# Kernel tuning notes

Hardware: AMD Instinct MI355X
Metric: run time of the kernel (lower is better)

Reference implementation:

```python
import jax, jax.numpy as jnp
import numpy as np

H, D = 8, 16          # heads, head dim -> out_channels = 128
L = 3                 # num GATv2 layers per graph stack
NUM_GRAPHS = 128      # pooled batch size
NEG_SLOPE = 0.2       # GATv2 leaky_relu slope


def _gatv2_stack(x, edge_index, eattr, linlW, linlb, linrW, linrb, lineW, att, bias, resW, resb):
    # x: [N, C]; edge_index: [2, E]; eattr: [E, edge_dim]
    src, dst = edge_index[0], edge_index[1]
    N = x.shape[0]
    for l in range(L):
        xl = (x @ linlW[l] + linlb[l]).reshape(N, H, D)   # source transform
        xr = (x @ linrW[l] + linrb[l]).reshape(N, H, D)   # target transform
        em = (eattr @ lineW[l]).reshape(-1, H, D)         # edge transform
        m = jax.nn.leaky_relu(xl[src] + xr[dst] + em, NEG_SLOPE)   # [E, H, D]
        logits = jnp.einsum('ehd,hd->eh', m, att[l])                # [E, H]
        # segment softmax over destination nodes (numerically stable)
        lmax = jax.ops.segment_max(logits, dst, num_segments=N)
        lmax = jnp.where(jnp.isfinite(lmax), lmax, 0.0)
        ex = jnp.exp(logits - lmax[dst])
        denom = jax.ops.segment_sum(ex, dst, num_segments=N)
        alpha = ex / (denom[dst] + 1e-16)
        agg = jax.ops.segment_sum(alpha[..., None] * xl[src], dst, num_segments=N)
        h = agg.reshape(N, H * D) + bias[l]               # GATv2Conv output
        x = h + jax.nn.elu(h @ resW[l] + resb[l])         # residual Linear+ELU block
    return x


def reference(mg_x, pg_x, mg_eattr, pg_eattr,
              mg_linlW, mg_linlb, mg_linrW, mg_linrb, mg_lineW, mg_att, mg_bias, mg_resW, mg_resb,
              pg_linlW, pg_linlb, pg_linrW, pg_linrb, pg_lineW, pg_att, pg_bias, pg_resW, pg_resb,
              fc1W, fc1b, fc2W, fc2b,
              mg_edge_index, pg_edge_index, mg_batch, pg_batch):
    mg_h = _gatv2_stack(mg_x, mg_edge_index, mg_eattr, mg_linlW, mg_linlb, mg_linrW, mg_linrb,
                        mg_lineW, mg_att, mg_bias, mg_resW, mg_resb)
    pg_h = _gatv2_stack(pg_x, pg_edge_index, pg_eattr, pg_linlW, pg_linlb, pg_linrW, pg_linrb,
                        pg_lineW, pg_att, pg_bias, pg_resW, pg_resb)
    mg_pool = jax.ops.segment_sum(mg_h, mg_batch, num_segments=NUM_GRAPHS)  # global_add_pool
    pg_pool = jax.ops.segment_sum(pg_h, pg_batch, num_segments=NUM_GRAPHS)
    z = jnp.concatenate([mg_pool, pg_pool], axis=-1)      # [B, 256]
    z = jax.nn.elu(z @ fc1W + fc1b)
    return jax.nn.sigmoid(z @ fc2W + fc2b)                # [B, 1]


def setup_inputs() -> dict:
    key = jax.random.key(0)
    ks = jax.random.split(key, 24)
    NM, NP = 50000, 20000          # molecule / protein node counts
    EM, EP = 400000, 400000        # edge counts
    EDM, EDP = 8, 12               # edge feature dims
    C = H * D                      # 128 = out_channels
    s = 0.05
    rn = lambda k, sh: jax.random.normal(k, sh, dtype=jnp.float32)
    return {
        "mg_x": rn(ks[0], (NM, C)),
        "pg_x": rn(ks[1], (NP, C)),
        "mg_eattr": rn(ks[2], (EM, EDM)),
        "pg_eattr": rn(ks[3], (EP, EDP)),
        "mg_linlW": rn(ks[4], (L, C, C)) * s,
        "mg_linlb": jnp.zeros((L, C), jnp.float32),
        "mg_linrW": rn(ks[5], (L, C, C)) * s,
        "mg_linrb": jnp.zeros((L, C), jnp.float32),
        "mg_lineW": rn(ks[6], (L, EDM, C)) * s,
        "mg_att": rn(ks[7], (L, H, D)) * s,
        "mg_bias": jnp.zeros((L, C), jnp.float32),
        "mg_resW": rn(ks[8], (L, C, C)) * s,
        "mg_resb": jnp.zeros((L, C), jnp.float32),
        "pg_linlW": rn(ks[9], (L, C, C)) * s,
        "pg_linlb": jnp.zeros((L, C), jnp.float32),
        "pg_linrW": rn(ks[10], (L, C, C)) * s,
        "pg_linrb": jnp.zeros((L, C), jnp.float32),
        "pg_lineW": rn(ks[11], (L, EDP, C)) * s,
        "pg_att": rn(ks[12], (L, H, D)) * s,
        "pg_bias": jnp.zeros((L, C), jnp.float32),
        "pg_resW": rn(ks[13], (L, C, C)) * s,
        "pg_resb": jnp.zeros((L, C), jnp.float32),
        "fc1W": rn(ks[14], (2 * C, C)) * s,
        "fc1b": jnp.zeros((C,), jnp.float32),
        "fc2W": rn(ks[15], (C, 1)) * s,
        "fc2b": jnp.zeros((1,), jnp.float32),
        "mg_edge_index": jax.random.randint(ks[16], (2, EM), 0, NM, dtype=jnp.int32),
        "pg_edge_index": jax.random.randint(ks[17], (2, EP), 0, NP, dtype=jnp.int32),
        "mg_batch": jnp.sort(jax.random.randint(ks[18], (NM,), 0, NUM_GRAPHS, dtype=jnp.int32)),
        "pg_batch": jnp.sort(jax.random.randint(ks[19], (NP,), 0, NUM_GRAPHS, dtype=jnp.int32)),
    }
```

## Files before the change

kernel.cpp:

```cpp
#include <hip/hip_runtime.h>
#include <hip/hip_bf16.h>

#define CDIM 128
#define NG 128
typedef unsigned int uint32;
typedef unsigned short ushort16;
typedef __attribute__((ext_vector_type(8))) short short8;
typedef __attribute__((ext_vector_type(4))) float floatx4;

__device__ __forceinline__ ushort16 f2bf(float f){
  uint32 u = __float_as_uint(f);
  u = (u + 0x7fffu + ((u >> 16) & 1u)) >> 16;
  return (ushort16)u;
}

__global__ void k_count_f(const int* __restrict__ dstM, const int* __restrict__ dstP,
                          int* __restrict__ deg, int EM, int ET, int NM){
  int e = blockIdx.x*blockDim.x + threadIdx.x;
  if (e < ET){
    int d = (e < EM) ? dstM[e] : dstP[e-EM] + NM;
    atomicAdd(&deg[d], 1);
  }
}

__global__ void k_scan1(const int* __restrict__ deg, int* __restrict__ rowptr,
                        int* __restrict__ sums, int N){
  __shared__ int tmp[1024];
  int b = blockIdx.x, t = threadIdx.x;
  int i = b*1024 + t;
  int v = (i < N) ? deg[i] : 0;
  tmp[t] = v; __syncthreads();
  for (int off = 1; off < 1024; off <<= 1){
    int a = (t >= off) ? tmp[t-off] : 0;
    __syncthreads();
    tmp[t] += a;
    __syncthreads();
  }
  if (i < N) rowptr[i] = tmp[t] - v;
  if (t == 1023) sums[b] = tmp[t];
}

__global__ void k_scan2(int* __restrict__ sums, int nb){
  __shared__ int tmp[1024];
  __shared__ int carry;
  int t = threadIdx.x;
  if (t == 0) carry = 0;
  __syncthreads();
  for (int base = 0; base < nb; base += 1024){
    int i = base + t;
    int v = (i < nb) ? sums[i] : 0;
    tmp[t] = v; __syncthreads();
    for (int off = 1; off < 1024; off <<= 1){
      int a = (t >= off) ? tmp[t-off] : 0;
      __syncthreads();
      tmp[t] += a;
      __syncthreads();
    }
    if (i < nb) sums[i] = carry + tmp[t] - v;
    int tot = tmp[1023];
    __syncthreads();
    if (t == 0) carry += tot;
    __syncthreads();
  }
  if (t == 0) sums[nb] = carry;
}

__global__ void k_scan3(int* __restrict__ rowptr, int* __restrict__ cursor,
                        const int* __restrict__ sums, int N, int nb){
  int i = blockIdx.x*blockDim.x + threadIdx.x;
  if (i < N){
    int r = rowptr[i] + sums[i >> 10];
    rowptr[i] = r; cursor[i] = r;
  }
  if (i == 0) rowptr[N] = sums[nb];
}

__global__ void k_scatter_f(const int* __restrict__ srcM, const int* __restrict__ srcP,
                            const int* __restrict__ dstM, const int* __restrict__ dstP,
                            int* __restrict__ cursor, int* __restrict__ csr_src,
                            int* __restrict__ csr_eid, int EM, int ET, int NM){
  int e = blockIdx.x*blockDim.x + threadIdx.x;
  if (e < ET){
    int s, d;
    if (e < EM){ s = srcM[e]; d = dstM[e]; }
    else       { s = srcP[e-EM] + NM; d = dstP[e-EM] + NM; }
    int pos = atomicAdd(&cursor[d], 1);
    csr_src[pos] = s;
    csr_eid[pos] = e;
  }
}

__global__ void k_reorder_f(const float* __restrict__ eaM, const float* __restrict__ eaP,
                            const int* __restrict__ eid, float* __restrict__ ea_csr,
                            int EM, int ET, int edM, int edP, int edmax){
  int i = blockIdx.x*blockDim.x + threadIdx.x;
  if (i >= ET*edmax) return;
  int j = i/edmax, k = i - j*edmax;
  if (j < EM){
    if (k < edM) ea_csr[(size_t)j*edM + k] = eaM[(size_t)eid[j]*edM + k];
  } else {
    if (k < edP) ea_csr[(size_t)EM*edM + (size_t)(j-EM)*edP + k]
                 = eaP[(size_t)(eid[j]-EM)*edP + k];
  }
}

__global__ void k_prep_w(const float* __restrict__ linlW_M, const float* __restrict__ linrW_M,
                         const float* __restrict__ resW_M,
                         const float* __restrict__ linlW_P, const float* __restrict__ linrW_P,
                         const float* __restrict__ resW_P,
                         ushort16* __restrict__ WtAll, ushort16* __restrict__ resWt){
  const int per = 256*CDIM + CDIM*CDIM;
  int idx = blockIdx.x*blockDim.x + threadIdx.x;
  if (idx >= 6*per) return;
  int sl = idx / per; int rem = idx - sl*per;
  int s = sl / 3, l = sl % 3;
  const float* Wl = (s ? linlW_P : linlW_M) + (size_t)l*CDIM*CDIM;
  const float* Wr = (s ? linrW_P : linrW_M) + (size_t)l*CDIM*CDIM;
  const float* Rw = (s ? resW_P  : resW_M ) + (size_t)l*CDIM*CDIM;
  if (rem < 256*CDIM){
    int k = rem >> 8, n = rem & 255;
    float v = (n < CDIM) ? Wl[k*CDIM + n] : Wr[k*CDIM + (n-CDIM)];
    WtAll[((size_t)sl*256 + n)*CDIM + k] = f2bf(v);
  } else {
    int r2 = rem - 256*CDIM;
    int k = r2 >> 7, n = r2 & 127;
    resWt[((size_t)sl*CDIM + n)*CDIM + k] = f2bf(Rw[k*CDIM + n]);
  }
}

__global__ void __launch_bounds__(256, 6)
k_transform_mfma(const float* __restrict__ xM, const float* __restrict__ xP,
    const ushort16* __restrict__ WtM, const ushort16* __restrict__ WtP,
    const float* __restrict__ blM, const float* __restrict__ brM,
    const float* __restrict__ blP, const float* __restrict__ brP,
    ushort16* __restrict__ xlh, float* __restrict__ xr,
    int NM, int nb32M, int NP)
{
  __shared__ ushort16 xs[32*CDIM];
  __shared__ float   xro[32*CDIM];
  int tid = threadIdx.x;
  int b = blockIdx.x;
  const float* xin; const ushort16* Wt; const float *bl, *br;
  int n0, nn, outbase;
  if (b < nb32M){ xin=xM; n0=b*32; nn=min(32,NM-n0); outbase=n0; Wt=WtM; bl=blM; br=brM; }
  else { xin=xP; n0=(b-nb32M)*32; nn=min(32,NP-n0); outbase=NM+n0; Wt=WtP; bl=blP; br=brP; }
  for (int i = 0; i < 16; i++){
    int e = tid + i*256;
    int row = e >> 7, col = e & 127;
    float v = (row < nn) ? xin[(size_t)(n0+row)*CDIM + col] : 0.f;
    int byte = (row*256 + col*2) ^ ((row & 7) << 4);
    *(ushort16*)((char*)xs + byte) = f2bf(v);
  }
  __syncthreads();
  int w = tid >> 6, t = tid & 63;
  int r16 = t & 15, kg = t >> 4;
  floatx4 acc[2][4];
  #pragma unroll
  for (int m = 0; m < 2; m++)
    #pragma unroll
    for (int nb = 0; nb < 4; nb++) acc[m][nb] = (floatx4){0.f,0.f,0.f,0.f};
  #pragma unroll
  for (int ks = 0; ks < 4; ks++){
    short8 a[2];
    #pragma unroll
    for (int m = 0; m < 2; m++){
      int row = m*16 + r16;
      int byte = (row*256 + ks*64 + kg*16) ^ ((row & 7) << 4);
      a[m] = *(const short8*)((const char*)xs + byte);
    }
    #pragma unroll
    for (int nb = 0; nb < 4; nb++){
      int col = w*64 + nb*16 + r16;
      short8 bf = *(const short8*)(Wt + (size_t)col*CDIM + ks*32 + kg*8);
      #pragma unroll
      for (int m = 0; m < 2; m++)
        acc[m][nb] = __builtin_amdgcn_mfma_f32_16x16x32_bf16(a[m], bf, acc[m][nb], 0, 0, 0);
    }
  }
  __syncthreads();
  #pragma unroll
  for (int nb = 0; nb < 4; nb++){
    int col = w*64 + nb*16 + r16;
    float bias = (col < CDIM) ? bl[col] : br[col - CDIM];
    #pragma unroll
    for (int m = 0; m < 2; m++){
      #pragma unroll
      for (int reg = 0; reg < 4; reg++){
        int row = m*16 + kg*4 + reg;
        float v = acc[m][nb][reg] + bias;
        if (col < CDIM) xs[row*CDIM + col] = f2bf(v);
        else            xro[row*CDIM + (col - CDIM)] = v;
      }
    }
  }
  __syncthreads();
  for (int i = 0; i < 16; i++){
    int e = tid + i*256;
    int row = e >> 7, col = e & 127;
    if (row < nn){
      xlh[(size_t)(outbase+row)*CDIM + col] = xs[e];
      xr [(size_t)(outbase+row)*CDIM + col] = xro[e];
    }
  }
}

template<int ED>
__device__ __forceinline__ void gat_edges(
    int start, int end, int t, int j0, int ed_rt,
    const uint32* __restrict__ xlu, float2 xrv, float2 at2,
    const float2* __restrict__ lw2,
    const float* __restrict__ ea, const int* __restrict__ eid,
    const int* __restrict__ csr_src,
    float& m, float& den, float& a0, float& a1)
{
  const int ed = (ED > 0) ? ED : ed_rt;
  for (int j = start; j < end; j += 4){
    const int r = end - j;
    int jj1 = (1 < r) ? j+1 : j;
    int jj2 = (2 < r) ? j+2 : j;
    int jj3 = (3 < r) ? j+3 : j;
    int s0 = __builtin_amdgcn_readfirstlane(csr_src[j]);
    int s1 = __builtin_amdgcn_readfirstlane(csr_src[jj1]);
    int s2 = __builtin_amdgcn_readfirstlane(csr_src[jj2]);
    int s3 = __builtin_amdgcn_readfirstlane(csr_src[jj3]);
    int e0 = __builtin_amdgcn_readfirstlane((eid ? eid[j]   : j)   - j0);
    int e1 = __builtin_amdgcn_readfirstlane((eid ? eid[jj1] : jj1) - j0);
    int e2 = __builtin_amdgcn_readfirstlane((eid ? eid[jj2] : jj2) - j0);
    int e3 = __builtin_amdgcn_readfirstlane((eid ? eid[jj3] : jj3) - j0);
    const float* p0 = ea + (size_t)e0*ed;
    const float* p1 = ea + (size_t)e1*ed;
    const float* p2 = ea + (size_t)e2*ed;
    const float* p3 = ea + (size_t)e3*ed;
    uint32 u0 = xlu[(size_t)s0*64 + t];
    uint32 u1 = xlu[(size_t)s1*64 + t];
    uint32 u2 = xlu[(size_t)s2*64 + t];
    uint32 u3 = xlu[(size_t)s3*64 + t];
    float x0x = __uint_as_float(u0 << 16), x0y = __uint_as_float(u0 & 0xffff0000u);
    float x1x = __uint_as_float(u1 << 16), x1y = __uint_as_float(u1 & 0xffff0000u);
    float x2x = __uint_as_float(u2 << 16), x2y = __uint_as_float(u2 & 0xffff0000u);
    float x3x = __uint_as_float(u3 << 16), x3y = __uint_as_float(u3 & 0xffff0000u);
    float em00=0.f, em01=0.f, em10=0.f, em11=0.f;
    float em20=0.f, em21=0.f, em30=0.f, em31=0.f;
    #pragma unroll 4
    for (int k = 0; k < ed; k++){
      float2 lwv = lw2[k*64 + t];
      float a = p0[k], bq = p1[k], c = p2[k], d = p3[k];
      em00 = fmaf(a,  lwv.x, em00); em01 = fmaf(a,  lwv.y, em01);
      em10 = fmaf(bq, lwv.x, em10); em11 = fmaf(bq, lwv.y, em11);
      em20 = fmaf(c,  lwv.x, em20); em21 = fmaf(c,  lwv.y, em21);
      em30 = fmaf(d,  lwv.x, em30); em31 = fmaf(d,  lwv.y, em31);
    }
    float m00 = x0x + xrv.x + em00; m00 = (m00>=0.f)?m00:0.2f*m00;
    float m01 = x0y + xrv.y + em01; m01 = (m01>=0.f)?m01:0.2f*m01;
    float m10 = x1x + xrv.x + em10; m10 = (m10>=0.f)?m10:0.2f*m10;
    float m11 = x1y + xrv.y + em11; m11 = (m11>=0.f)?m11:0.2f*m11;
    float m20 = x2x + xrv.x + em20; m20 = (m20>=0.f)?m20:0.2f*m20;
    float m21 = x2y + xrv.y + em21; m21 = (m21>=0.f)?m21:0.2f*m21;
    float m30 = x3x + xrv.x + em30; m30 = (m30>=0.f)?m30:0.2f*m30;
    float m31 = x3y + xrv.y + em31; m31 = (m31>=0.f)?m31:0.2f*m31;
    float v0 = fmaf(m00, at2.x, m01*at2.y);
    float v1 = fmaf(m10, at2.x, m11*at2.y);
    float v2 = fmaf(m20, at2.x, m21*at2.y);
    float v3 = fmaf(m30, at2.x, m31*at2.y);
    #pragma unroll
    for (int off = 1; off < 8; off <<= 1){
      v0 += __shfl_xor(v0, off, 8);
      v1 += __shfl_xor(v1, off, 8);
      v2 += __shfl_xor(v2, off, 8);
      v3 += __shfl_xor(v3, off, 8);
    }
    if (1 >= r) v1 = -INFINITY;
    if (2 >= r) v2 = -INFINITY;
    if (3 >= r) v3 = -INFINITY;
    float vmax = fmaxf(fmaxf(v0, v1), fmaxf(v2, v3));
    if (vmax > m + 8.f){
      float sc = __expf(m - vmax);
      den *= sc; a0 *= sc; a1 *= sc; m = vmax;
    }
    float w0 = __expf(v0 - m), w1 = __expf(v1 - m);
    float w2 = __expf(v2 - m), w3 = __expf(v3 - m);
    den += (w0 + w1) + (w2 + w3);
    a0 = fmaf(w0, x0x, fmaf(w1, x1x, fmaf(w2, x2x, fmaf(w3, x3x, a0))));
    a1 = fmaf(w0, x0y, fmaf(w1, x1y, fmaf(w2, x2y, fmaf(w3, x3y, a1))));
  }
}

template<int EDM_T, int EDP_T>
__global__ void __launch_bounds__(256, 8)
k_gat_f(const uint32* __restrict__ xlu, const float2* __restrict__ xr2,
    const float* __restrict__ eaM, const float* __restrict__ eaP,
    const int* __restrict__ eid,
    const float* __restrict__ lwM, const float* __restrict__ atM, const float* __restrict__ biM,
    const float* __restrict__ lwP, const float* __restrict__ atP, const float* __restrict__ biP,
    const int* __restrict__ rowptr, const int* __restrict__ csr_src,
    float2* __restrict__ hout2, int NM, int NT, int EM, int edM_rt, int edP_rt)
{
  const int edM = (EDM_T > 0) ? EDM_T : edM_rt;
  const int edP = (EDP_T > 0) ? EDP_T : edP_rt;
  __shared__ float lw[24*CDIM];
  int tb = threadIdx.x;
  for (int i = tb; i < edM*CDIM; i += 256) lw[i] = lwM[i];
  for (int i = tb; i < edP*CDIM; i += 256) lw[edM*CDIM + i] = lwP[i];
  __syncthreads();
  int w = tb >> 6;
  int t = tb & 63;
  const float2* lwM2 = (const float2*)lw;
  const float2* lwP2 = (const float2*)(lw + edM*CDIM);
  float2 at2M = ((const float2*)atM)[t];
  float2 at2P = ((const float2*)atP)[t];
  float2 bb2M = ((const float2*)biM)[t];
  float2 bb2P = ((const float2*)biP)[t];
  for (int n = blockIdx.x*4 + w; n < NT; n += gridDim.x*4){
    bool mg = (n < NM);
    float2 xrv = xr2[(size_t)n*64 + t];
    int start = __builtin_amdgcn_readfirstlane(rowptr[n]);
    int end   = __builtin_amdgcn_readfirstlane(rowptr[n+1]);
    float m = -INFINITY, den = 0.f, a0 = 0.f, a1 = 0.f;
    if (mg)
      gat_edges<EDM_T>(start, end, t, 0, edM, xlu, xrv, at2M, lwM2,
                       eaM, eid, csr_src, m, den, a0, a1);
    else
      gat_edges<EDP_T>(start, end, t, EM, edP, xlu, xrv, at2P, lwP2,
                       eaP, eid, csr_src, m, den, a0, a1);
    float2 bb2 = mg ? bb2M : bb2P;
    float inv = 1.f/(den + 1e-16f);
    hout2[(size_t)n*64 + t] = make_float2(fmaf(a0, inv, bb2.x), fmaf(a1, inv, bb2.y));
  }
}

__global__ void __launch_bounds__(256, 6)
k_epilogue_mfma(const float* __restrict__ hin,
    const ushort16* __restrict__ RtM, const ushort16* __restrict__ RtP,
    const float* __restrict__ RbM, const float* __restrict__ RbP,
    float* __restrict__ xout, int NM, int nb32M, int NP,
    const int* __restrict__ batchM, const int* __restrict__ batchP,
    float* __restrict__ pool, int dopool)
{
  __shared__ ushort16 hb[32*CDIM];
  __shared__ float hf[32*CDIM];
  int tid = threadIdx.x;
  int b = blockIdx.x;
  const ushort16* Rt; const float* Rb; const int* batch;
  int n0, nn, iobase, off;
  if (b < nb32M){ n0=b*32; nn=min(32,NM-n0); iobase=n0; Rt=RtM; Rb=RbM; batch=batchM; off=0; }
  else { n0=(b-nb32M)*32; nn=min(32,NP-n0); iobase=NM+n0; Rt=RtP; Rb=RbP; batch=batchP; off=CDIM; }
  for (int i = 0; i < 16; i++){
    int e = tid + i*256;
    int row = e >> 7, col = e & 127;
    float v = (row < nn) ? hin[(size_t)(iobase+row)*CDIM + col] : 0.f;
    hf[e] = v;
    int byte = (row*256 + col*2) ^ ((row & 7) << 4);
    *(ushort16*)((char*)hb + byte) = f2bf(v);
  }
  __syncthreads();
  int w = tid >> 6, t = tid & 63;
  int r16 = t & 15, kg = t >> 4;
  floatx4 acc[2][2];
  #pragma unroll
  for (int m = 0; m < 2; m++)
    #pragma unroll
    for (int nb = 0; nb < 2; nb++) acc[m][nb] = (floatx4){0.f,0.f,0.f,0.f};
  #pragma unroll
  for (int ks = 0; ks < 4; ks++){
    short8 a[2];
    #pragma unroll
    for (int m = 0; m < 2; m++){
      int row = m*16 + r16;
      int byte = (row*256 + ks*64 + kg*16) ^ ((row & 7) << 4);
      a[m] = *(const short8*)((const char*)hb + byte);
    }
    #pragma unroll
    for (int nb = 0; nb < 2; nb++){
      int col = w*32 + nb*16 + r16;
      short8 bf = *(const short8*)(Rt + (size_t)col*CDIM + ks*32 + kg*8);
      #pragma unroll
      for (int m = 0; m < 2; m++)
        acc[m][nb] = __builtin_amdgcn_mfma_f32_16x16x32_bf16(a[m], bf, acc[m][nb], 0, 0, 0);
    }
  }
  #pragma unroll
  for (int nb = 0; nb < 2; nb++){
    int col = w*32 + nb*16 + r16;
    float rb = Rb[col];
    #pragma unroll
    for (int m = 0; m < 2; m++){
      #pragma unroll
      for (int reg = 0; reg < 4; reg++){
        int row = m*16 + kg*4 + reg;
        float r = acc[m][nb][reg] + rb;
        float e = (r > 0.f) ? r : expm1f(r);
        hf[row*CDIM + col] = hf[row*CDIM + col] + e;
      }
    }
  }
  __syncthreads();
  for (int i = 0; i < 16; i++){
    int e = tid + i*256;
    int row = e >> 7, col = e & 127;
    if (row < nn){
      float val = hf[e];
      if (dopool){
        int g = batch[n0 + row];
        atomicAdd(&pool[(size_t)g*256 + off + col], val);
      } else {
        xout[(size_t)(iobase+row)*CDIM + col] = val;
      }
    }
  }
}

__global__ void k_head(const float* __restrict__ pool,
    const float* __restrict__ fc1W, const float* __restrict__ fc1b,
    const float* __restrict__ fc2W, const float* __restrict__ fc2b,
    float* __restrict__ out)
{
  __shared__ float ps[256];
  __shared__ float zs[CDIM];
  int g = blockIdx.x, t = threadIdx.x;
  ps[t]       = pool[g*256 + t];
  ps[t + 128] = pool[g*256 + 128 + t];
  __syncthreads();
  float acc = 0.f;
  for (int k = 0; k < 256; k++) acc = fmaf(ps[k], fc1W[k*CDIM + t], acc);
  acc += fc1b[t];
  float z = (acc > 0.f) ? acc : expm1f(acc);
  zs[t] = z * fc2W[t];
  __syncthreads();
  for (int s = 64; s > 0; s >>= 1){
    if (t < s) zs[t] += zs[t + s];
    __syncthreads();
  }
  if (t == 0){
    float o = zs[0] + fc2b[0];
    out[g] = 1.f / (1.f + expf(-o));
  }
}

extern "C" void kernel_launch(void* const* d_in, const int* in_sizes, int n_in,
                              void* d_out, int out_size, void* d_ws, size_t ws_size,
                              hipStream_t stream)
{
  const int NM = in_sizes[0] / CDIM, NP = in_sizes[1] / CDIM;
  const int EM = in_sizes[26] / 2,   EP = in_sizes[27] / 2;
  const int edM = in_sizes[2] / EM,  edP = in_sizes[3] / EP;
  const int NT = NM + NP, ET = EM + EP;
  const int edmax = (edM > edP) ? edM : edP;

  const int nb32M = (NM + 31)/32, nb32P = (NP + 31)/32;
  const int nbT32 = nb32M + nb32P;
  const int nbScan = (NT + 1023)/1024;

  float* Wp = (float*)d_ws;
  float* x      = Wp;
  ushort16* xlh = (ushort16*)(x + (size_t)NT*CDIM);
  float* xr     = (float*)(xlh) + (size_t)NT*64;
  float* pool   = xr + (size_t)NT*CDIM;
  int* rowptr  = (int*)(pool + (size_t)NG*256);
  int* deg     = rowptr + NT + 1;
  int* cursor  = deg + NT;
  int* sums    = cursor + NT;
  int* csr_src = sums + nbScan + 1;
  int* csr_eid = csr_src + ET;
  float* ea_csr = (float*)(csr_eid + ET);
  size_t ea_elems = (size_t)EM*edM + (size_t)EP*edP;
  ushort16* WtAll = (ushort16*)(ea_csr + ea_elems);
  ushort16* resWt = WtAll + (size_t)6*256*CDIM;

  size_t need = ((size_t)NT*CDIM + (size_t)NT*64 + (size_t)NT*CDIM + (size_t)NG*256)*4
              + ((size_t)3*NT + 1 + nbScan + 1 + (size_t)2*ET)*4
              + ea_elems*4
              + ((size_t)6*256*CDIM + (size_t)6*CDIM*CDIM)*2;
  if (ws_size < need) return;

  const float* xM0    = (const float*)d_in[0];
  const float* xP0    = (const float*)d_in[1];
  const float* eattrM = (const float*)d_in[2];
  const float* eattrP = (const float*)d_in[3];
  const int* eiM = (const int*)d_in[26];
  const int* eiP = (const int*)d_in[27];
  const int* batchM = (const int*)d_in[28];
  const int* batchP = (const int*)d_in[29];
  const int* srcM = eiM, *dstM = eiM + EM;
  const int* srcP = eiP, *dstP = eiP + EP;

  hipMemsetAsync(pool, 0, (size_t)NG*256*sizeof(float), stream);
  hipMemsetAsync(deg, 0, (size_t)NT*sizeof(int), stream);

  {
    const int tot = 6*(256*CDIM + CDIM*CDIM);
    k_prep_w<<<(tot + 255)/256, 256, 0, stream>>>(
        (const float*)d_in[4], (const float*)d_in[6], (const float*)d_in[11],
        (const float*)d_in[13], (const float*)d_in[15], (const float*)d_in[20],
        WtAll, resWt);
  }

  k_count_f<<<(ET + 255)/256, 256, 0, stream>>>(dstM, dstP, deg, EM, ET, NM);
  k_scan1<<<nbScan, 1024, 0, stream>>>(deg, rowptr, sums, NT);
  k_scan2<<<1, 1024, 0, stream>>>(sums, nbScan);
  k_scan3<<<(NT + 255)/256, 256, 0, stream>>>(rowptr, cursor, sums, NT, nbScan);
  k_scatter_f<<<(ET + 255)/256, 256, 0, stream>>>(srcM, srcP, dstM, dstP, cursor,
                                                  csr_src, csr_eid, EM, ET, NM);
  k_reorder_f<<<((size_t)ET*edmax + 255)/256, 256, 0, stream>>>(
      eattrM, eattrP, csr_eid, ea_csr, EM, ET, edM, edP, edmax);
  const float* eaM_use = ea_csr;
  const float* eaP_use = ea_csr + (size_t)EM*edM;

  int gatBlocks = (NT + 3)/4;
  if (gatBlocks > 2048) gatBlocks = 2048;

  for (int l = 0; l < 3; l++){
    const float* blM = (const float*)d_in[5]  + (size_t)l*CDIM;
    const float* brM = (const float*)d_in[7]  + (size_t)l*CDIM;
    const float* WeM = (const float*)d_in[8]  + (size_t)l*edM*CDIM;
    const float* atM = (const float*)d_in[9]  + (size_t)l*CDIM;
    const float* biM = (const float*)d_in[10] + (size_t)l*CDIM;
    const float* RbM = (const float*)d_in[12] + (size_t)l*CDIM;
    const float* blP = (const float*)d_in[14] + (size_t)l*CDIM;
    const float* brP = (const float*)d_in[16] + (size_t)l*CDIM;
    const float* WeP = (const float*)d_in[17] + (size_t)l*edP*CDIM;
    const float* atP = (const float*)d_in[18] + (size_t)l*CDIM;
    const float* biP = (const float*)d_in[19] + (size_t)l*CDIM;
    const float* RbP = (const float*)d_in[21] + (size_t)l*CDIM;

    const ushort16* WtM_l = WtAll + ((size_t)(0*3 + l))*256*CDIM;
    const ushort16* WtP_l = WtAll + ((size_t)(1*3 + l))*256*CDIM;
    const ushort16* RtM_l = resWt + ((size_t)(0*3 + l))*CDIM*CDIM;
    const ushort16* RtP_l = resWt + ((size_t)(1*3 + l))*CDIM*CDIM;

    const float* xMin = (l == 0) ? xM0 : x;
    const float* xPin = (l == 0) ? xP0 : x + (size_t)NM*CDIM;

    k_transform_mfma<<<nbT32, 256, 0, stream>>>(xMin, xPin, WtM_l, WtP_l,
        blM, brM, blP, brP, xlh, xr, NM, nb32M, NP);

    if (edM == 8 && edP == 12)
      k_gat_f<8,12><<<gatBlocks, 256, 0, stream>>>((const uint32*)xlh, (const float2*)xr,
          eaM_use, eaP_use, nullptr, WeM, atM, biM, WeP, atP, biP,
          rowptr, csr_src, (float2*)xr, NM, NT, EM, edM, edP);
    else
      k_gat_f<0,0><<<gatBlocks, 256, 0, stream>>>((const uint32*)xlh, (const float2*)xr,
          eaM_use, eaP_use, nullptr, WeM, atM, biM, WeP, atP, biP,
          rowptr, csr_src, (float2*)xr, NM, NT, EM, edM, edP);

    k_epilogue_mfma<<<nbT32, 256, 0, stream>>>(xr, RtM_l, RtP_l, RbM, RbP, x,
        NM, nb32M, NP, batchM, batchP, pool, (l == 2) ? 1 : 0);
  }

  const float* fc1W = (const float*)d_in[22];
  const float* fc1b = (const float*)d_in[23];
  const float* fc2W = (const float*)d_in[24];
  const float* fc2b = (const float*)d_in[25];
  k_head<<<NG, 128, 0, stream>>>(pool, fc1W, fc1b, fc2W, fc2b, (float*)d_out);
}
```

Baseline: 644.6 us.

## Fuse residual epilogue with next-layer transform and prefetch next edge batch in GAT

Adds a kernel that applies the residual Linear+ELU and then, in the same block, runs the next layer's source/target transform. The intermediate x no longer makes a global round trip, and one launch per layer is removed. The GAT edge loop is also software-pipelined: the next four source indices and xl rows are loaded before the current batch is computed, to hide gather latency. The unused eid path is dropped, and the final epilogue now always pools. The cost is higher register and LDS pressure in the fused kernel, and the prefetch may lower occupancy.

```diff
diff --git a/kernel.cpp b/kernel.cpp
--- a/kernel.cpp
+++ b/kernel.cpp
@@ -204,41 +204,188 @@
   }
 }
 
+__global__ void __launch_bounds__(256, 6)
+k_fused_et(const float* __restrict__ hin,
+    const ushort16* __restrict__ RtM, const ushort16* __restrict__ RtP,
+    const float* __restrict__ RbM, const float* __restrict__ RbP,
+    const ushort16* __restrict__ WtM, const ushort16* __restrict__ WtP,
+    const float* __restrict__ blM, const float* __restrict__ brM,
+    const float* __restrict__ blP, const float* __restrict__ brP,
+    ushort16* __restrict__ xlh, float* __restrict__ xr,
+    int NM, int nb32M, int NP)
+{
+  __shared__ ushort16 ab[32*CDIM];
+  __shared__ float    hf[32*CDIM];
+  int tid = threadIdx.x;
+  int b = blockIdx.x;
+  const ushort16 *Rt, *Wt; const float *Rb, *bl, *br;
+  int n0, nn, iobase;
+  if (b < nb32M){ n0=b*32; nn=min(32,NM-n0); iobase=n0;
+    Rt=RtM; Rb=RbM; Wt=WtM; bl=blM; br=brM; }
+  else { n0=(b-nb32M)*32; nn=min(32,NP-n0); iobase=NM+n0;
+    Rt=RtP; Rb=RbP; Wt=WtP; bl=blP; br=brP; }
+  for (int i = 0; i < 16; i++){
+    int e = tid + i*256;
+    int row = e >> 7, col = e & 127;
+    float v = (row < nn) ? hin[(size_t)(iobase+row)*CDIM + col] : 0.f;
+    hf[e] = v;
+    int byte = (row*256 + col*2) ^ ((row & 7) << 4);
+    *(ushort16*)((char*)ab + byte) = f2bf(v);
+  }
+  __syncthreads();
+  int w = tid >> 6, t = tid & 63;
+  int r16 = t & 15, kg = t >> 4;
+  floatx4 acc1[2][2];
+  #pragma unroll
+  for (int m = 0; m < 2; m++)
+    #pragma unroll
+    for (int nb = 0; nb < 2; nb++) acc1[m][nb] = (floatx4){0.f,0.f,0.f,0.f};
+  #pragma unroll
+  for (int ks = 0; ks < 4; ks++){
+    short8 a[2];
+    #pragma unroll
+    for (int m = 0; m < 2; m++){
+      int row = m*16 + r16;
+      int byte = (row*256 + ks*64 + kg*16) ^ ((row & 7) << 4);
+      a[m] = *(const short8*)((const char*)ab + byte);
+    }
+    #pragma unroll
+    for (int nb = 0; nb < 2; nb++){
+      int col = w*32 + nb*16 + r16;
+      short8 bf = *(const short8*)(Rt + (size_t)col*CDIM + ks*32 + kg*8);
+      #pragma unroll
+      for (int m = 0; m < 2; m++)
+        acc1[m][nb] = __builtin_amdgcn_mfma_f32_16x16x32_bf16(a[m], bf, acc1[m][nb], 0, 0, 0);
+    }
+  }
+  __syncthreads();
+  #pragma unroll
+  for (int nb = 0; nb < 2; nb++){
+    int col = w*32 + nb*16 + r16;
+    float rb = Rb[col];
+    #pragma unroll
+    for (int m = 0; m < 2; m++){
+      #pragma unroll
+      for (int reg = 0; reg < 4; reg++){
+        int row = m*16 + kg*4 + reg;
+        float r = acc1[m][nb][reg] + rb;
+        float e = (r > 0.f) ? r : expm1f(r);
+        float xv = hf[row*CDIM + col] + e;
+        hf[row*CDIM + col] = xv;
+        int byte = (row*256 + col*2) ^ ((row & 7) << 4);
+        *(ushort16*)((char*)ab + byte) = f2bf(xv);
+      }
+    }
+  }
+  __syncthreads();
+  floatx4 acc2[2][4];
+  #pragma unroll
+  for (int m = 0; m < 2; m++)
+    #pragma unroll
+    for (int nb = 0; nb < 4; nb++) acc2[m][nb] = (floatx4){0.f,0.f,0.f,0.f};
+  #pragma unroll
+  for (int ks = 0; ks < 4; ks++){
+    short8 a[2];
+    #pragma unroll
+    for (int m = 0; m < 2; m++){
+      int row = m*16 + r16;
+      int byte = (row*256 + ks*64 + kg*16) ^ ((row & 7) << 4);
+      a[m] = *(const short8*)((const char*)ab + byte);
+    }
+    #pragma unroll
+    for (int nb = 0; nb < 4; nb++){
+      int col = w*64 + nb*16 + r16;
+      short8 bf = *(const short8*)(Wt + (size_t)col*CDIM + ks*32 + kg*8);
+      #pragma unroll
+      for (int m = 0; m < 2; m++)
+        acc2[m][nb] = __builtin_amdgcn_mfma_f32_16x16x32_bf16(a[m], bf, acc2[m][nb], 0, 0, 0);
+    }
+  }
+  __syncthreads();
+  #pragma unroll
+  for (int nb = 0; nb < 4; nb++){
+    int col = w*64 + nb*16 + r16;
+    float bias = (col < CDIM) ? bl[col] : br[col - CDIM];
+    #pragma unroll
+    for (int m = 0; m < 2; m++){
+      #pragma unroll
+      for (int reg = 0; reg < 4; reg++){
+        int row = m*16 + kg*4 + reg;
+        float v = acc2[m][nb][reg] + bias;
+        if (col < CDIM) ab[row*CDIM + col] = f2bf(v);
+        else            hf[row*CDIM + (col - CDIM)] = v;
+      }
+    }
+  }
+  __syncthreads();
+  for (int i = 0; i < 16; i++){
+    int e = tid + i*256;
+    int row = e >> 7, col = e & 127;
+    if (row < nn){
+      xlh[(size_t)(iobase+row)*CDIM + col] = ab[e];
+      xr [(size_t)(iobase+row)*CDIM + col] = hf[e];
+    }
+  }
+}
+
 template<int ED>
 __device__ __forceinline__ void gat_edges(
     int start, int end, int t, int j0, int ed_rt,
     const uint32* __restrict__ xlu, float2 xrv, float2 at2,
     const float2* __restrict__ lw2,
-    const float* __restrict__ ea, const int* __restrict__ eid,
-    const int* __restrict__ csr_src,
+    const float* __restrict__ ea, const int* __restrict__ csr_src,
     float& m, float& den, float& a0, float& a1)
 {
   const int ed = (ED > 0) ? ED : ed_rt;
-  for (int j = start; j < end; j += 4){
-    const int r = end - j;
-    int jj1 = (1 < r) ? j+1 : j;
-    int jj2 = (2 < r) ? j+2 : j;
-    int jj3 = (3 < r) ? j+3 : j;
-    int s0 = __builtin_amdgcn_readfirstlane(csr_src[j]);
-    int s1 = __builtin_amdgcn_readfirstlane(csr_src[jj1]);
-    int s2 = __builtin_amdgcn_readfirstlane(csr_src[jj2]);
-    int s3 = __builtin_amdgcn_readfirstlane(csr_src[jj3]);
-    int e0 = __builtin_amdgcn_readfirstlane((eid ? eid[j]   : j)   - j0);
-    int e1 = __builtin_amdgcn_readfirstlane((eid ? eid[jj1] : jj1) - j0);
-    int e2 = __builtin_amdgcn_readfirstlane((eid ? eid[jj2] : jj2) - j0);
-    int e3 = __builtin_amdgcn_readfirstlane((eid ? eid[jj3] : jj3) - j0);
-    const float* p0 = ea + (size_t)e0*ed;
-    const float* p1 = ea + (size_t)e1*ed;
-    const float* p2 = ea + (size_t)e2*ed;
-    const float* p3 = ea + (size_t)e3*ed;
-    uint32 u0 = xlu[(size_t)s0*64 + t];
-    uint32 u1 = xlu[(size_t)s1*64 + t];
-    uint32 u2 = xlu[(size_t)s2*64 + t];
-    uint32 u3 = xlu[(size_t)s3*64 + t];
-    float x0x = __uint_as_float(u0 << 16), x0y = __uint_as_float(u0 & 0xffff0000u);
-    float x1x = __uint_as_float(u1 << 16), x1y = __uint_as_float(u1 & 0xffff0000u);
-    float x2x = __uint_as_float(u2 << 16), x2y = __uint_as_float(u2 & 0xffff0000u);
-    float x3x = __uint_as_float(u3 << 16), x3y = __uint_as_float(u3 & 0xffff0000u);
+  if (start >= end) return;
+  int j = start;
+  int r = end - j;
+  int jj1 = (1 < r) ? j+1 : j;
+  int jj2 = (2 < r) ? j+2 : j;
+  int jj3 = (3 < r) ? j+3 : j;
+  int e0 = __builtin_amdgcn_readfirstlane(j   - j0);
+  int e1 = __builtin_amdgcn_readfirstlane(jj1 - j0);
+  int e2 = __builtin_amdgcn_readfirstlane(jj2 - j0);
+  int e3 = __builtin_amdgcn_readfirstlane(jj3 - j0);
+  int s0 = __builtin_amdgcn_readfirstlane(csr_src[j]);
+  int s1 = __builtin_amdgcn_readfirstlane(csr_src[jj1]);
+  int s2 = __builtin_amdgcn_readfirstlane(csr_src[jj2]);
+  int s3 = __builtin_amdgcn_readfirstlane(csr_src[jj3]);
+  uint32 u0 = xlu[(size_t)s0*64 + t];
+  uint32 u1 = xlu[(size_t)s1*64 + t];
+  uint32 u2 = xlu[(size_t)s2*64 + t];
+  uint32 u3 = xlu[(size_t)s3*64 + t];
+  while (j < end){
+    uint32 c0 = u0, c1 = u1, c2 = u2, c3 = u3;
+    int ce0 = e0, ce1 = e1, ce2 = e2, ce3 = e3;
+    int cr = r;
+    int nj = j + 4;
+    if (nj < end){
+      r = end - nj;
+      jj1 = (1 < r) ? nj+1 : nj;
+      jj2 = (2 < r) ? nj+2 : nj;
+      jj3 = (3 < r) ? nj+3 : nj;
+      e0 = __builtin_amdgcn_readfirstlane(nj  - j0);
+      e1 = __builtin_amdgcn_readfirstlane(jj1 - j0);
+      e2 = __builtin_amdgcn_readfirstlane(jj2 - j0);
+      e3 = __builtin_amdgcn_readfirstlane(jj3 - j0);
+      s0 = __builtin_amdgcn_readfirstlane(csr_src[nj]);
+      s1 = __builtin_amdgcn_readfirstlane(csr_src[jj1]);
+      s2 = __builtin_amdgcn_readfirstlane(csr_src[jj2]);
+      s3 = __builtin_amdgcn_readfirstlane(csr_src[jj3]);
+      u0 = xlu[(size_t)s0*64 + t];
+      u1 = xlu[(size_t)s1*64 + t];
+      u2 = xlu[(size_t)s2*64 + t];
+      u3 = xlu[(size_t)s3*64 + t];
+    }
+    const float* p0 = ea + (size_t)ce0*ed;
+    const float* p1 = ea + (size_t)ce1*ed;
+    const float* p2 = ea + (size_t)ce2*ed;
+    const float* p3 = ea + (size_t)ce3*ed;
+    float x0x = __uint_as_float(c0 << 16), x0y = __uint_as_float(c0 & 0xffff0000u);
+    float x1x = __uint_as_float(c1 << 16), x1y = __uint_as_float(c1 & 0xffff0000u);
+    float x2x = __uint_as_float(c2 << 16), x2y = __uint_as_float(c2 & 0xffff0000u);
+    float x3x = __uint_as_float(c3 << 16), x3y = __uint_as_float(c3 & 0xffff0000u);
     float em00=0.f, em01=0.f, em10=0.f, em11=0.f;
     float em20=0.f, em21=0.f, em30=0.f, em31=0.f;
     #pragma unroll 4
@@ -269,9 +416,9 @@
       v2 += __shfl_xor(v2, off, 8);
       v3 += __shfl_xor(v3, off, 8);
     }
-    if (1 >= r) v1 = -INFINITY;
-    if (2 >= r) v2 = -INFINITY;
-    if (3 >= r) v3 = -INFINITY;
+    if (1 >= cr) v1 = -INFINITY;
+    if (2 >= cr) v2 = -INFINITY;
+    if (3 >= cr) v3 = -INFINITY;
     float vmax = fmaxf(fmaxf(v0, v1), fmaxf(v2, v3));
     if (vmax > m + 8.f){
       float sc = __expf(m - vmax);
@@ -282,6 +429,7 @@
     den += (w0 + w1) + (w2 + w3);
     a0 = fmaf(w0, x0x, fmaf(w1, x1x, fmaf(w2, x2x, fmaf(w3, x3x, a0))));
     a1 = fmaf(w0, x0y, fmaf(w1, x1y, fmaf(w2, x2y, fmaf(w3, x3y, a1))));
+    j = nj;
   }
 }
 
@@ -289,7 +437,6 @@
 __global__ void __launch_bounds__(256, 8)
 k_gat_f(const uint32* __restrict__ xlu, const float2* __restrict__ xr2,
     const float* __restrict__ eaM, const float* __restrict__ eaP,
-    const int* __restrict__ eid,
     const float* __restrict__ lwM, const float* __restrict__ atM, const float* __restrict__ biM,
     const float* __restrict__ lwP, const float* __restrict__ atP, const float* __restrict__ biP,
     const int* __restrict__ rowptr, const int* __restrict__ csr_src,
@@ -318,10 +465,10 @@
     float m = -INFINITY, den = 0.f, a0 = 0.f, a1 = 0.f;
     if (mg)
       gat_edges<EDM_T>(start, end, t, 0, edM, xlu, xrv, at2M, lwM2,
-                       eaM, eid, csr_src, m, den, a0, a1);
+                       eaM, csr_src, m, den, a0, a1);
     else
       gat_edges<EDP_T>(start, end, t, EM, edP, xlu, xrv, at2P, lwP2,
-                       eaP, eid, csr_src, m, den, a0, a1);
+                       eaP, csr_src, m, den, a0, a1);
     float2 bb2 = mg ? bb2M : bb2P;
     float inv = 1.f/(den + 1e-16f);
     hout2[(size_t)n*64 + t] = make_float2(fmaf(a0, inv, bb2.x), fmaf(a1, inv, bb2.y));
@@ -332,9 +479,9 @@
 k_epilogue_mfma(const float* __restrict__ hin,
     const ushort16* __restrict__ RtM, const ushort16* __restrict__ RtP,
     const float* __restrict__ RbM, const float* __restrict__ RbP,
-    float* __restrict__ xout, int NM, int nb32M, int NP,
+    int NM, int nb32M, int NP,
     const int* __restrict__ batchM, const int* __restrict__ batchP,
-    float* __restrict__ pool, int dopool)
+    float* __restrict__ pool)
 {
   __shared__ ushort16 hb[32*CDIM];
   __shared__ float hf[32*CDIM];
@@ -398,13 +545,8 @@
     int e = tid + i*256;
     int row = e >> 7, col = e & 127;
     if (row < nn){
-      float val = hf[e];
-      if (dopool){
-        int g = batch[n0 + row];
-        atomicAdd(&pool[(size_t)g*256 + off + col], val);
-      } else {
-        xout[(size_t)(iobase+row)*CDIM + col] = val;
-      }
+      int g = batch[n0 + row];
+      atomicAdd(&pool[(size_t)g*256 + off + col], hf[e]);
     }
   }
 }
@@ -508,43 +650,43 @@
   int gatBlocks = (NT + 3)/4;
   if (gatBlocks > 2048) gatBlocks = 2048;
 
-  for (int l = 0; l < 3; l++){
-    const float* blM = (const float*)d_in[5]  + (size_t)l*CDIM;
-    const float* brM = (const float*)d_in[7]  + (size_t)l*CDIM;
+  auto runGat = [&](int l){
     const float* WeM = (const float*)d_in[8]  + (size_t)l*edM*CDIM;
     const float* atM = (const float*)d_in[9]  + (size_t)l*CDIM;
     const float* biM = (const float*)d_in[10] + (size_t)l*CDIM;
-    const float* RbM = (const float*)d_in[12] + (size_t)l*CDIM;
-    const float* blP = (const float*)d_in[14] + (size_t)l*CDIM;
-    const float* brP = (const float*)d_in[16] + (size_t)l*CDIM;
     const float* WeP = (const float*)d_in[17] + (size_t)l*edP*CDIM;
     const float* atP = (const float*)d_in[18] + (size_t)l*CDIM;
     const float* biP = (const float*)d_in[19] + (size_t)l*CDIM;
-    const float* RbP = (const float*)d_in[21] + (size_t)l*CDIM;
-
-    const ushort16* WtM_l = WtAll + ((size_t)(0*3 + l))*256*CDIM;
-    const ushort16* WtP_l = WtAll + ((size_t)(1*3 + l))*256*CDIM;
-    const ushort16* RtM_l = resWt + ((size_t)(0*3 + l))*CDIM*CDIM;
-    const ushort16* RtP_l = resWt + ((size_t)(1*3 + l))*CDIM*CDIM;
-
-    const float* xMin = (l == 0) ? xM0 : x;
-    const float* xPin = (l == 0) ? xP0 : x + (size_t)NM*CDIM;
-
-    k_transform_mfma<<<nbT32, 256, 0, stream>>>(xMin, xPin, WtM_l, WtP_l,
-        blM, brM, blP, brP, xlh, xr, NM, nb32M, NP);
-
     if (edM == 8 && edP == 12)
       k_gat_f<8,12><<<gatBlocks, 256, 0, stream>>>((const uint32*)xlh, (const float2*)xr,
-          eaM_use, eaP_use, nullptr, WeM, atM, biM, WeP, atP, biP,
+          eaM_use, eaP_use, WeM, atM, biM, WeP, atP, biP,
           rowptr, csr_src, (float2*)xr, NM, NT, EM, edM, edP);
     else
       k_gat_f<0,0><<<gatBlocks, 256, 0, stream>>>((const uint32*)xlh, (const float2*)xr,
-          eaM_use, eaP_use, nullptr, WeM, atM, biM, WeP, atP, biP,
+          eaM_use, eaP_use, WeM, atM, biM, WeP, atP, biP,
           rowptr, csr_src, (float2*)xr, NM, NT, EM, edM, edP);
-
-    k_epilogue_mfma<<<nbT32, 256, 0, stream>>>(xr, RtM_l, RtP_l, RbM, RbP, x,
-        NM, nb32M, NP, batchM, batchP, pool, (l == 2) ? 1 : 0);
-  }
+  };
+
+  k_transform_mfma<<<nbT32, 256, 0, stream>>>(xM0, xP0,
+      WtAll + 0*(size_t)256*CDIM, WtAll + 3*(size_t)256*CDIM,
+      (const float*)d_in[5], (const float*)d_in[7],
+      (const float*)d_in[14], (const float*)d_in[16],
+      xlh, xr, NM, nb32M, NP);
+  runGat(0);
+  for (int l = 0; l < 2; l++){
+    k_fused_et<<<nbT32, 256, 0, stream>>>(xr,
+        resWt + (size_t)(0*3 + l)*CDIM*CDIM, resWt + (size_t)(1*3 + l)*CDIM*CDIM,
+        (const float*)d_in[12] + (size_t)l*CDIM, (const float*)d_in[21] + (size_t)l*CDIM,
+        WtAll + (size_t)(0*3 + l+1)*256*CDIM, WtAll + (size_t)(1*3 + l+1)*256*CDIM,
+        (const float*)d_in[5]  + (size_t)(l+1)*CDIM, (const float*)d_in[7]  + (size_t)(l+1)*CDIM,
+        (const float*)d_in[14] + (size_t)(l+1)*CDIM, (const float*)d_in[16] + (size_t)(l+1)*CDIM,
+        xlh, xr, NM, nb32M, NP);
+    runGat(l+1);
+  }
+  k_epilogue_mfma<<<nbT32, 256, 0, stream>>>(xr,
+      resWt + (size_t)(0*3 + 2)*CDIM*CDIM, resWt + (size_t)(1*3 + 2)*CDIM*CDIM,
+      (const float*)d_in[12] + (size_t)2*CDIM, (const float*)d_in[21] + (size_t)2*CDIM,
+      NM, nb32M, NP, batchM, batchP, pool);
 
   const float* fc1W = (const float*)d_in[22];
   const float* fc1b = (const float*)d_in[23];
```

New measurement: 701.6 us. 1.09x slower.
